# Kernel tuning notes

Measured on AMD Instinct MI355X. Metric: run time of the kernel, lower is better.

The kernel has to match this reference:

```python
import jax, jax.numpy as jnp
import numpy as np

NUM_ENT = 14541
NUM_REL = 474
D = 400
B = 32
N_CAND = 14505


def setup_inputs() -> dict:
    key = jax.random.key(0)
    k0, k1, k2, k4, k5 = jax.random.split(key, 5)
    return {
        "arg0_1": jax.random.normal(k0, (NUM_ENT, D), dtype=jnp.float32),   # entity embeddings
        "arg1_1": jax.random.normal(k1, (NUM_REL, D), dtype=jnp.float32),   # relation centers
        "arg2_1": jax.random.uniform(k2, (NUM_REL, D), dtype=jnp.float32),  # relation offsets (box widths)
        "arg3_1": jnp.ones((1,), dtype=jnp.float32),                        # margin gamma
        "arg4_1": jax.random.randint(k4, (B, 2), 0, NUM_REL),               # (head_id, rel_id) pairs
        "arg5_1": jax.random.randint(k5, (4, N_CAND), 0, NUM_ENT),          # candidate entity ids (row 0 used)
    }


def reference(arg0_1, arg1_1, arg2_1, arg3_1, arg4_1, arg5_1):
    # Gather heads / relation params
    head = arg0_1[arg4_1[:, 0]]            # [B, D]
    rel_c = arg1_1[arg4_1[:, 1]]           # [B, D]
    rel_o = arg2_1[arg4_1[:, 1]]           # [B, D]

    query = (head + rel_c)[:, None, :]     # [B, 1, D] box center
    offset = rel_o[:, None, :]             # [B, 1, D] box width

    # Candidate tail embeddings: only row 0 of arg5_1 is used in the graph
    cand = arg0_1[arg5_1[0].reshape(-1)][None, :, :]  # [1, N_CAND, D]

    d = jnp.abs(cand - query)                           # [B, N_CAND, D]
    dist_outside = jax.nn.relu(d - offset).sum(-1)      # [B, N_CAND]
    dist_inside = jnp.abs(jnp.minimum(d, offset)).sum(-1)

    return arg3_1 - dist_outside - 0.02 * dist_inside   # [B, N_CAND]
```

## Files before the change

### kernel.cpp

```cpp
#include <hip/hip_runtime.h>

#define DIM     400
#define NENT    14541
#define B       32
#define NCAND   14505
#define NSTRIP  303
#define DROWS   14544
#define CVTN    (DROWS * 50)
#define CVTBLK  ((CVTN + 255) / 256)
#define THREADS 256

typedef __attribute__((ext_vector_type(2))) _Float16 half2_t;

static __device__ __forceinline__ half2_t bch(unsigned u) {
    return __builtin_bit_cast(half2_t, u);
}
static __device__ __forceinline__ half2_t habs2(half2_t x) {
    unsigned u = __builtin_bit_cast(unsigned, x) & 0x7fff7fffu;
    return __builtin_bit_cast(half2_t, u);
}
static __device__ __forceinline__ unsigned pkh(float x, float y) {
    half2_t h;
    h.x = (_Float16)x;
    h.y = (_Float16)y;
    return __builtin_bit_cast(unsigned, h);
}
static __device__ __forceinline__ float dot2acc(half2_t m, float s) {
#if __has_builtin(__builtin_amdgcn_fdot2)
    const half2_t ones = {(_Float16)1.f, (_Float16)1.f};
    return __builtin_amdgcn_fdot2(m, ones, s, false);
#else
    return s + (float)m.x + (float)m.y;
#endif
}

__global__ void setup_kernel(const float* __restrict__ ent,
                             const float* __restrict__ relc,
                             const float* __restrict__ relo,
                             const float* __restrict__ onev,
                             const int*   __restrict__ pairs,
                             const int*   __restrict__ cidx,
                             uint4* __restrict__ dense16,
                             _Float16* __restrict__ q16,
                             _Float16* __restrict__ o16,
                             float* __restrict__ baseg) {
    const int blk = blockIdx.x;
    const int tid = threadIdx.x;
    if (blk < CVTBLK) {
        int i = blk * THREADS + tid;
        if (i >= CVTN) return;
        int row = i / 50;
        int col = i - row * 50;
        int n  = row < NCAND ? row : NCAND - 1;
        int ci = cidx[n];
        const float4* s4 = (const float4*)(ent + (size_t)ci * DIM) + col * 2;
        float4 a = s4[0], c = s4[1];
        uint4 d;
        d.x = pkh(a.x, a.y);
        d.y = pkh(a.z, a.w);
        d.z = pkh(c.x, c.y);
        d.w = pkh(c.z, c.w);
        dense16[i] = d;
    } else {
        const int b = blk - CVTBLK;
        const int h = pairs[2 * b + 0];
        const int r = pairs[2 * b + 1];
        float so = 0.f;
        for (int i = tid; i < DIM; i += THREADS) {
            float qv = ent[(size_t)h * DIM + i] + relc[(size_t)r * DIM + i];
            float ov = relo[(size_t)r * DIM + i];
            q16[(size_t)b * DIM + i] = (_Float16)qv;
            o16[(size_t)b * DIM + i] = (_Float16)(0.98f * ov);
            so += ov;
        }
        __shared__ float sred[4];
        for (int off = 32; off; off >>= 1) so += __shfl_down(so, off);
        if ((tid & 63) == 0) sred[tid >> 6] = so;
        __syncthreads();
        if (tid == 0)
            baseg[b] = onev[0] + 0.98f * (sred[0] + sred[1] + sred[2] + sred[3]);
    }
}

__global__ __launch_bounds__(THREADS, 2)
void score_f16(const uint4* __restrict__ dense16,
               const uint4* __restrict__ q16,
               const uint4* __restrict__ o16,
               const float* __restrict__ baseg,
               float* __restrict__ out) {
    const int fid  = blockIdx.x;
    const int xcd  = fid & 7;
    const int rest = fid >> 3;
    const int bq   = rest & 7;
    const int tc   = rest >> 3;
    const int strip = xcd + 8 * tc;
    if (strip >= NSTRIP) return;

    const int r0 = strip * 12;
    const int r1 = r0 + 12;

    const int tid  = threadIdx.x;
    const int wid  = tid >> 6;
    const int lane = tid & 63;
    const int u    = lane & 15;
    const int g    = lane >> 4;
    const int b    = __builtin_amdgcn_readfirstlane(4 * bq + wid);

    const uint4* qa = q16 + (size_t)b * 50;
    const uint4* oa = o16 + (size_t)b * 50;
    uint4 q[4], o[4];
    q[0] = qa[u]; q[1] = qa[u + 16]; q[2] = qa[u + 32];
    o[0] = oa[u]; o[1] = oa[u + 16]; o[2] = oa[u + 32];
    q[3] = q[0]; o[3] = o[0];
    if (u < 2) { q[3] = qa[48 + u]; o[3] = oa[48 + u]; }
    const float base = baseg[b];

    const half2_t K002 = {(_Float16)0.02f, (_Float16)0.02f};

#define PAIR(cu, qu, ou, SS)                                    \
    {                                                           \
        half2_t cc_ = bch(cu), qq_ = bch(qu), oo_ = bch(ou);    \
        half2_t dd_ = cc_ - qq_;                                \
        half2_t aa_ = habs2(dd_);                               \
        half2_t ee_ = aa_ * K002 + oo_;                         \
        half2_t mm_ = __builtin_elementwise_max(aa_, ee_);      \
        SS = dot2acc(mm_, SS);                                  \
    }
#define PROC(C, Q, O, SA, SB)                                   \
    PAIR(C.x, Q.x, O.x, SA) PAIR(C.y, Q.y, O.y, SB)             \
    PAIR(C.z, Q.z, O.z, SA) PAIR(C.w, Q.w, O.w, SB)

    for (int rr = r0; rr < r1; rr += 3) {
        const uint4* pA = dense16 + (size_t)(4 * rr + g) * 50;
        const uint4* pB = pA + 200;
        const uint4* pC = pA + 400;

        uint4 av0 = pA[u], av1 = pA[u + 16], av2 = pA[u + 32];
        uint4 bv0 = pB[u], bv1 = pB[u + 16], bv2 = pB[u + 32];
        uint4 cv0 = pC[u], cv1 = pC[u + 16], cv2 = pC[u + 32];
        uint4 av3, bv3, cv3;
        if (u < 2) { av3 = pA[48 + u]; bv3 = pB[48 + u]; cv3 = pC[48 + u]; }

        float sA0 = 0.f, sA1 = 0.f, sB0 = 0.f, sB1 = 0.f, sC0 = 0.f, sC1 = 0.f;
        PROC(av0, q[0], o[0], sA0, sA1)
        PROC(av1, q[1], o[1], sA0, sA1)
        PROC(av2, q[2], o[2], sA0, sA1)
        if (u < 2) { PROC(av3, q[3], o[3], sA0, sA1) }
        PROC(bv0, q[0], o[0], sB0, sB1)
        PROC(bv1, q[1], o[1], sB0, sB1)
        PROC(bv2, q[2], o[2], sB0, sB1)
        if (u < 2) { PROC(bv3, q[3], o[3], sB0, sB1) }
        PROC(cv0, q[0], o[0], sC0, sC1)
        PROC(cv1, q[1], o[1], sC0, sC1)
        PROC(cv2, q[2], o[2], sC0, sC1)
        if (u < 2) { PROC(cv3, q[3], o[3], sC0, sC1) }

        float sA = sA0 + sA1;
        float sB = sB0 + sB1;
        float sC = sC0 + sC1;
        sA += __shfl_xor(sA, 1); sB += __shfl_xor(sB, 1); sC += __shfl_xor(sC, 1);
        sA += __shfl_xor(sA, 2); sB += __shfl_xor(sB, 2); sC += __shfl_xor(sC, 2);
        sA += __shfl_xor(sA, 4); sB += __shfl_xor(sB, 4); sC += __shfl_xor(sC, 4);
        sA += __shfl_xor(sA, 8); sB += __shfl_xor(sB, 8); sC += __shfl_xor(sC, 8);

        if (u == 0) {
            const int candA = 4 * rr + g;
            if (candA < NCAND)     out[(size_t)b * NCAND + candA]     = base - sA;
            if (candA + 4 < NCAND) out[(size_t)b * NCAND + candA + 4] = base - sB;
            if (candA + 8 < NCAND) out[(size_t)b * NCAND + candA + 8] = base - sC;
        }
    }
#undef PROC
#undef PAIR
}

__global__ __launch_bounds__(THREADS, 2)
void score_f32(const float* __restrict__ ent,
               const float* __restrict__ relc,
               const float* __restrict__ relo,
               const float* __restrict__ onev,
               const int*   __restrict__ pairs,
               const int*   __restrict__ cidx,
               float* __restrict__ out) {
    const int fid  = blockIdx.x;
    const int xcd  = fid & 7;
    const int rest = fid >> 3;
    const int bq   = rest & 7;
    const int tc   = rest >> 3;
    const int t    = xcd + 8 * tc;

    const int tid  = threadIdx.x;
    const int lane = tid & 63;
    const int u    = lane & 15;
    const int g    = lane >> 4;
    const int b    = __builtin_amdgcn_readfirstlane(bq * 4 + (tid >> 6));

    const int hd = pairs[b * 2 + 0];
    const int rl = pairs[b * 2 + 1];
    const float4* hb = (const float4*)(ent  + (size_t)hd * DIM) + u;
    const float4* cb = (const float4*)(relc + (size_t)rl * DIM) + u;
    const float4* ob = (const float4*)(relo + (size_t)rl * DIM) + u;

    float4 q[7], o[7];
    float oa = 0.f;
#pragma unroll
    for (int k = 0; k < 6; ++k) {
        float4 h = hb[16 * k], c = cb[16 * k];
        q[k] = make_float4(h.x + c.x, h.y + c.y, h.z + c.z, h.w + c.w);
        o[k] = ob[16 * k];
        oa += o[k].x + o[k].y + o[k].z + o[k].w;
    }
    if (u < 4) {
        float4 h = hb[96], c = cb[96];
        q[6] = make_float4(h.x + c.x, h.y + c.y, h.z + c.z, h.w + c.w);
        o[6] = ob[96];
        oa += o[6].x + o[6].y + o[6].z + o[6].w;
    }
    oa += __shfl_xor(oa, 1);
    oa += __shfl_xor(oa, 2);
    oa += __shfl_xor(oa, 4);
    oa += __shfl_xor(oa, 8);
    const float base = onev[0] + 0.98f * oa;

    const float4* entu = (const float4*)ent + u;

#define E(vc, vq, vo, AM, AD)                     \
        {                                         \
            float d_ = (vc) - (vq);               \
            AM += fmaxf(fabsf(d_), (vo));         \
            AD += fabsf(d_);                      \
        }
#define F4(k, AM, AD)                             \
        E(cbuf[k].x, q[k].x, o[k].x, AM, AD)      \
        E(cbuf[k].y, q[k].y, o[k].y, AM, AD)      \
        E(cbuf[k].z, q[k].z, o[k].z, AM, AD)      \
        E(cbuf[k].w, q[k].w, o[k].w, AM, AD)

    for (int rr = t; rr < 3627; rr += 256) {
        const int cand = 4 * rr + g;
        const int ci   = cidx[cand < NCAND ? cand : NCAND - 1];
        const float4* p = entu + (size_t)ci * 100;

        float4 cbuf[7];
#pragma unroll
        for (int k = 0; k < 6; ++k) cbuf[k] = p[16 * k];
        if (u < 4) cbuf[6] = p[96];

        float am0 = 0.f, ad0 = 0.f, am1 = 0.f, ad1 = 0.f;
        F4(0, am0, ad0) F4(1, am1, ad1)
        F4(2, am0, ad0) F4(3, am1, ad1)
        F4(4, am0, ad0) F4(5, am1, ad1)
        if (u < 4) { F4(6, am0, ad0) }

        float s_ = fmaf(-0.98f, am0 + am1, -0.02f * (ad0 + ad1));
        s_ += __shfl_xor(s_, 1);
        s_ += __shfl_xor(s_, 2);
        s_ += __shfl_xor(s_, 4);
        s_ += __shfl_xor(s_, 8);

        if (u == 0 && cand < NCAND)
            out[(size_t)b * NCAND + cand] = base + s_;
    }
#undef F4
#undef E
}

extern "C" void kernel_launch(void* const* d_in, const int* in_sizes, int n_in,
                              void* d_out, int out_size, void* d_ws, size_t ws_size,
                              hipStream_t stream) {
    const float* ent   = (const float*)d_in[0];
    const float* relc  = (const float*)d_in[1];
    const float* relo  = (const float*)d_in[2];
    const float* onev  = (const float*)d_in[3];
    const int*   pairs = (const int*)d_in[4];
    const int*   cidx  = (const int*)d_in[5];
    float*       out   = (float*)d_out;

    const size_t denB = (size_t)DROWS * DIM * 2;
    const size_t qB   = (size_t)B * DIM * 2;
    const size_t need = denB + 2 * qB + B * sizeof(float);

    if (ws_size >= need) {
        unsigned char* w = (unsigned char*)d_ws;
        uint4*    dense16 = (uint4*)w;
        _Float16* q16     = (_Float16*)(w + denB);
        _Float16* o16     = (_Float16*)(w + denB + qB);
        float*    baseg   = (float*)(w + denB + 2 * qB);

        setup_kernel<<<CVTBLK + B, THREADS, 0, stream>>>(
            ent, relc, relo, onev, pairs, cidx, dense16, q16, o16, baseg);
        score_f16<<<8 * 8 * 38, THREADS, 0, stream>>>(
            dense16, (const uint4*)q16, (const uint4*)o16, baseg, out);
    } else {
        score_f32<<<8 * 8 * 32, THREADS, 0, stream>>>(
            ent, relc, relo, onev, pairs, cidx, out);
    }
}
```

Baseline: 39.84 us.

## Map lanes to batch queries with LDS-staged transposed query/offset tables

Query and offset vectors are now written in a transposed [chunk][batch] layout and staged into shared memory by every scoring block. Each wavefront lane handles one batch row against one candidate and loops over the full dimension, so the cross-lane shuffle reduction and per-lane query registers go away. Each lane now reads its own candidate row, while the 32 lanes sharing a candidate hit the same addresses and can be served by broadcast. The costs are a 51KB shared-memory fill in every block, which limits occupancy, and a longer serial per-lane loop. The block count is also rebuilt around candidate pairs instead of the XCD-aware strip mapping.

```diff
diff --git a/kernel.cpp b/kernel.cpp
--- a/kernel.cpp
+++ b/kernel.cpp
@@ -4,10 +4,11 @@
 #define NENT    14541
 #define B       32
 #define NCAND   14505
-#define NSTRIP  303
-#define DROWS   14544
+#define PAIRS   7280
+#define DROWS   14560
 #define CVTN    (DROWS * 50)
 #define CVTBLK  ((CVTN + 255) / 256)
+#define SBLOCKS (PAIRS / 8)
 #define THREADS 256
 
 typedef __attribute__((ext_vector_type(2))) _Float16 half2_t;
@@ -41,8 +42,8 @@
                              const int*   __restrict__ pairs,
                              const int*   __restrict__ cidx,
                              uint4* __restrict__ dense16,
-                             _Float16* __restrict__ q16,
-                             _Float16* __restrict__ o16,
+                             uint4* __restrict__ q16t,
+                             uint4* __restrict__ o16t,
                              float* __restrict__ baseg) {
     const int blk = blockIdx.x;
     const int tid = threadIdx.x;
@@ -66,58 +67,64 @@
         const int h = pairs[2 * b + 0];
         const int r = pairs[2 * b + 1];
         float so = 0.f;
-        for (int i = tid; i < DIM; i += THREADS) {
-            float qv = ent[(size_t)h * DIM + i] + relc[(size_t)r * DIM + i];
-            float ov = relo[(size_t)r * DIM + i];
-            q16[(size_t)b * DIM + i] = (_Float16)qv;
-            o16[(size_t)b * DIM + i] = (_Float16)(0.98f * ov);
-            so += ov;
-        }
-        __shared__ float sred[4];
-        for (int off = 32; off; off >>= 1) so += __shfl_down(so, off);
-        if ((tid & 63) == 0) sred[tid >> 6] = so;
-        __syncthreads();
-        if (tid == 0)
-            baseg[b] = onev[0] + 0.98f * (sred[0] + sred[1] + sred[2] + sred[3]);
+        if (tid < 50) {
+            const float4* hp = (const float4*)(ent  + (size_t)h * DIM) + 2 * tid;
+            const float4* cp = (const float4*)(relc + (size_t)r * DIM) + 2 * tid;
+            const float4* op = (const float4*)(relo + (size_t)r * DIM) + 2 * tid;
+            float4 h0 = hp[0], h1 = hp[1];
+            float4 c0 = cp[0], c1 = cp[1];
+            float4 v0 = op[0], v1 = op[1];
+            uint4 qv, ov;
+            qv.x = pkh(h0.x + c0.x, h0.y + c0.y);
+            qv.y = pkh(h0.z + c0.z, h0.w + c0.w);
+            qv.z = pkh(h1.x + c1.x, h1.y + c1.y);
+            qv.w = pkh(h1.z + c1.z, h1.w + c1.w);
+            ov.x = pkh(0.98f * v0.x, 0.98f * v0.y);
+            ov.y = pkh(0.98f * v0.z, 0.98f * v0.w);
+            ov.z = pkh(0.98f * v1.x, 0.98f * v1.y);
+            ov.w = pkh(0.98f * v1.z, 0.98f * v1.w);
+            q16t[tid * 32 + b] = qv;
+            o16t[tid * 32 + b] = ov;
+            so = v0.x + v0.y + v0.z + v0.w + v1.x + v1.y + v1.z + v1.w;
+        }
+        if (tid < 64) {
+            so += __shfl_xor(so, 1);
+            so += __shfl_xor(so, 2);
+            so += __shfl_xor(so, 4);
+            so += __shfl_xor(so, 8);
+            so += __shfl_xor(so, 16);
+            so += __shfl_xor(so, 32);
+            if (tid == 0) baseg[b] = onev[0] + 0.98f * so;
+        }
     }
 }
 
 __global__ __launch_bounds__(THREADS, 2)
 void score_f16(const uint4* __restrict__ dense16,
-               const uint4* __restrict__ q16,
-               const uint4* __restrict__ o16,
+               const uint4* __restrict__ q16t,
+               const uint4* __restrict__ o16t,
                const float* __restrict__ baseg,
                float* __restrict__ out) {
-    const int fid  = blockIdx.x;
-    const int xcd  = fid & 7;
-    const int rest = fid >> 3;
-    const int bq   = rest & 7;
-    const int tc   = rest >> 3;
-    const int strip = xcd + 8 * tc;
-    if (strip >= NSTRIP) return;
-
-    const int r0 = strip * 12;
-    const int r1 = r0 + 12;
-
-    const int tid  = threadIdx.x;
+    __shared__ uint4 qs[1600];
+    __shared__ uint4 os[1600];
+    const int tid = threadIdx.x;
+    for (int i = tid; i < 1600; i += THREADS) {
+        qs[i] = q16t[i];
+        os[i] = o16t[i];
+    }
+    __syncthreads();
+
     const int wid  = tid >> 6;
     const int lane = tid & 63;
-    const int u    = lane & 15;
-    const int g    = lane >> 4;
-    const int b    = __builtin_amdgcn_readfirstlane(4 * bq + wid);
-
-    const uint4* qa = q16 + (size_t)b * 50;
-    const uint4* oa = o16 + (size_t)b * 50;
-    uint4 q[4], o[4];
-    q[0] = qa[u]; q[1] = qa[u + 16]; q[2] = qa[u + 32];
-    o[0] = oa[u]; o[1] = oa[u + 16]; o[2] = oa[u + 32];
-    q[3] = q[0]; o[3] = o[0];
-    if (u < 2) { q[3] = qa[48 + u]; o[3] = oa[48 + u]; }
+    const int b    = lane & 31;
+    const int c2   = lane >> 5;
     const float base = baseg[b];
 
+    const int p0 = blockIdx.x * 8 + wid * 2;
+
     const half2_t K002 = {(_Float16)0.02f, (_Float16)0.02f};
 
-#define PAIR(cu, qu, ou, SS)                                    \
+#define PAIRE(cu, qu, ou, SS)                                   \
     {                                                           \
         half2_t cc_ = bch(cu), qq_ = bch(qu), oo_ = bch(ou);    \
         half2_t dd_ = cc_ - qq_;                                \
@@ -127,51 +134,33 @@
         SS = dot2acc(mm_, SS);                                  \
     }
 #define PROC(C, Q, O, SA, SB)                                   \
-    PAIR(C.x, Q.x, O.x, SA) PAIR(C.y, Q.y, O.y, SB)             \
-    PAIR(C.z, Q.z, O.z, SA) PAIR(C.w, Q.w, O.w, SB)
-
-    for (int rr = r0; rr < r1; rr += 3) {
-        const uint4* pA = dense16 + (size_t)(4 * rr + g) * 50;
-        const uint4* pB = pA + 200;
-        const uint4* pC = pA + 400;
-
-        uint4 av0 = pA[u], av1 = pA[u + 16], av2 = pA[u + 32];
-        uint4 bv0 = pB[u], bv1 = pB[u + 16], bv2 = pB[u + 32];
-        uint4 cv0 = pC[u], cv1 = pC[u + 16], cv2 = pC[u + 32];
-        uint4 av3, bv3, cv3;
-        if (u < 2) { av3 = pA[48 + u]; bv3 = pB[48 + u]; cv3 = pC[48 + u]; }
-
-        float sA0 = 0.f, sA1 = 0.f, sB0 = 0.f, sB1 = 0.f, sC0 = 0.f, sC1 = 0.f;
-        PROC(av0, q[0], o[0], sA0, sA1)
-        PROC(av1, q[1], o[1], sA0, sA1)
-        PROC(av2, q[2], o[2], sA0, sA1)
-        if (u < 2) { PROC(av3, q[3], o[3], sA0, sA1) }
-        PROC(bv0, q[0], o[0], sB0, sB1)
-        PROC(bv1, q[1], o[1], sB0, sB1)
-        PROC(bv2, q[2], o[2], sB0, sB1)
-        if (u < 2) { PROC(bv3, q[3], o[3], sB0, sB1) }
-        PROC(cv0, q[0], o[0], sC0, sC1)
-        PROC(cv1, q[1], o[1], sC0, sC1)
-        PROC(cv2, q[2], o[2], sC0, sC1)
-        if (u < 2) { PROC(cv3, q[3], o[3], sC0, sC1) }
-
-        float sA = sA0 + sA1;
-        float sB = sB0 + sB1;
-        float sC = sC0 + sC1;
-        sA += __shfl_xor(sA, 1); sB += __shfl_xor(sB, 1); sC += __shfl_xor(sC, 1);
-        sA += __shfl_xor(sA, 2); sB += __shfl_xor(sB, 2); sC += __shfl_xor(sC, 2);
-        sA += __shfl_xor(sA, 4); sB += __shfl_xor(sB, 4); sC += __shfl_xor(sC, 4);
-        sA += __shfl_xor(sA, 8); sB += __shfl_xor(sB, 8); sC += __shfl_xor(sC, 8);
-
-        if (u == 0) {
-            const int candA = 4 * rr + g;
-            if (candA < NCAND)     out[(size_t)b * NCAND + candA]     = base - sA;
-            if (candA + 4 < NCAND) out[(size_t)b * NCAND + candA + 4] = base - sB;
-            if (candA + 8 < NCAND) out[(size_t)b * NCAND + candA + 8] = base - sC;
-        }
+    PAIRE(C.x, Q.x, O.x, SA) PAIRE(C.y, Q.y, O.y, SB)           \
+    PAIRE(C.z, Q.z, O.z, SA) PAIRE(C.w, Q.w, O.w, SB)
+
+#pragma unroll
+    for (int pp = 0; pp < 2; ++pp) {
+        const int pair = p0 + pp;
+        const int cand = 2 * pair + c2;
+        const uint4* cp = dense16 + (size_t)cand * 50;
+
+        float s0 = 0.f, s1 = 0.f;
+#pragma unroll 5
+        for (int j = 0; j < 50; j += 2) {
+            uint4 cj0 = cp[j];
+            uint4 cj1 = cp[j + 1];
+            uint4 qj0 = qs[j * 32 + b];
+            uint4 oj0 = os[j * 32 + b];
+            uint4 qj1 = qs[(j + 1) * 32 + b];
+            uint4 oj1 = os[(j + 1) * 32 + b];
+            PROC(cj0, qj0, oj0, s0, s1)
+            PROC(cj1, qj1, oj1, s0, s1)
+        }
+
+        if (cand < NCAND)
+            out[(size_t)b * NCAND + cand] = base - (s0 + s1);
     }
 #undef PROC
-#undef PAIR
+#undef PAIRE
 }
 
 __global__ __launch_bounds__(THREADS, 2)
@@ -277,20 +266,20 @@
     float*       out   = (float*)d_out;
 
     const size_t denB = (size_t)DROWS * DIM * 2;
-    const size_t qB   = (size_t)B * DIM * 2;
+    const size_t qB   = (size_t)1600 * 16;
     const size_t need = denB + 2 * qB + B * sizeof(float);
 
     if (ws_size >= need) {
         unsigned char* w = (unsigned char*)d_ws;
-        uint4*    dense16 = (uint4*)w;
-        _Float16* q16     = (_Float16*)(w + denB);
-        _Float16* o16     = (_Float16*)(w + denB + qB);
-        float*    baseg   = (float*)(w + denB + 2 * qB);
+        uint4* dense16 = (uint4*)w;
+        uint4* q16t    = (uint4*)(w + denB);
+        uint4* o16t    = (uint4*)(w + denB + qB);
+        float* baseg   = (float*)(w + denB + 2 * qB);
 
         setup_kernel<<<CVTBLK + B, THREADS, 0, stream>>>(
-            ent, relc, relo, onev, pairs, cidx, dense16, q16, o16, baseg);
-        score_f16<<<8 * 8 * 38, THREADS, 0, stream>>>(
-            dense16, (const uint4*)q16, (const uint4*)o16, baseg, out);
+            ent, relc, relo, onev, pairs, cidx, dense16, q16t, o16t, baseg);
+        score_f16<<<SBLOCKS, THREADS, 0, stream>>>(
+            dense16, q16t, o16t, baseg, out);
     } else {
         score_f32<<<8 * 8 * 32, THREADS, 0, stream>>>(
             ent, relc, relo, onev, pairs, cidx, out);
```

Result: faster. 37.19 us (median of 2 runs) (-6.7%).
